# Performance work log

Hardware: AMD Instinct MI355X
Metric: run time of the kernel (lower is better)

Reference implementation:

```python
import jax, jax.numpy as jnp
import numpy as np

NUM_CLASSES = 80
NUM_ANCHORS = 9
NUM_CONVS = 4
FOCAL_ALPHA = 0.25
FOCAL_GAMMA = 2.0
LOSS_NORMALIZER = 100.0
LOSS_WEIGHT = 1.0
LEVEL_SHAPES = [(128, 128), (64, 64), (32, 32), (16, 16), (8, 8)]
C = 256
B = 2
N_TOTAL = NUM_ANCHORS * sum(h * w for h, w in LEVEL_SHAPES)  # 196416


def setup_inputs() -> dict:
    key = jax.random.key(0)
    ks = iter(jax.random.split(key, 32))
    inp = {}
    for i, (h, w) in enumerate(LEVEL_SHAPES):
        inp[f"feat{i}"] = jax.random.normal(next(ks), (B, h, w, C), dtype=jnp.float32)
    inp["anchor_labels"] = jax.random.randint(next(ks), (B, N_TOTAL), -1, NUM_CLASSES + 1, dtype=jnp.int32)
    inp["anchor_deltas"] = jax.random.normal(next(ks), (B, N_TOTAL, 4), dtype=jnp.float32)
    s = 0.05
    inp["in_proj_w"] = s * jax.random.normal(next(ks), (5, C, C), dtype=jnp.float32)  # [lvl, in, out]
    inp["in_proj_b"] = s * jax.random.normal(next(ks), (5, C), dtype=jnp.float32)
    inp["cls_convs_w"] = s * jax.random.normal(next(ks), (NUM_CONVS, 3, 3, C, C), dtype=jnp.float32)  # HWIO
    inp["cls_convs_b"] = s * jax.random.normal(next(ks), (NUM_CONVS, C), dtype=jnp.float32)
    inp["cls_score_w"] = s * jax.random.normal(next(ks), (3, 3, C, NUM_ANCHORS * NUM_CLASSES), dtype=jnp.float32)
    inp["cls_score_b"] = s * jax.random.normal(next(ks), (NUM_ANCHORS * NUM_CLASSES,), dtype=jnp.float32)
    inp["box_convs_w"] = s * jax.random.normal(next(ks), (NUM_CONVS, 3, 3, C, C), dtype=jnp.float32)
    inp["box_convs_b"] = s * jax.random.normal(next(ks), (NUM_CONVS, C), dtype=jnp.float32)
    inp["box_pred_w"] = s * jax.random.normal(next(ks), (3, 3, C, NUM_ANCHORS * 4), dtype=jnp.float32)
    inp["box_pred_b"] = s * jax.random.normal(next(ks), (NUM_ANCHORS * 4,), dtype=jnp.float32)
    return inp


def _conv(x, w, b):
    # x: [B,H,W,Cin] NHWC, w: [3,3,Cin,Cout] HWIO, stride 1, SAME padding
    y = jax.lax.conv_general_dilated(x, w, (1, 1), "SAME",
                                     dimension_numbers=("NHWC", "HWIO", "NHWC"))
    return y + b


def _head(feats, in_proj_w, in_proj_b, cls_convs_w, cls_convs_b, cls_score_w,
          cls_score_b, box_convs_w, box_convs_b, box_pred_w, box_pred_b):
    logit_maps, delta_maps = [], []
    for i, feat in enumerate(feats):  # fixed 5 FPN levels
        x = feat @ in_proj_w[i] + in_proj_b[i]  # in_proj Linear
        c = x
        for j in range(NUM_CONVS):
            c = jax.nn.relu(_conv(c, cls_convs_w[j], cls_convs_b[j]))
        logit = _conv(c, cls_score_w, cls_score_b)  # [B,H,W,A*K]
        d = x
        for j in range(NUM_CONVS):
            d = jax.nn.relu(_conv(d, box_convs_w[j], box_convs_b[j]))
        delta = _conv(d, box_pred_w, box_pred_b)  # [B,H,W,A*4]
        b, h, w, _ = logit.shape
        # reshape_pred_map: [B,H,W,A,P] -> [B, H*W*A, P] (channel c = a*P + p matches NHWC)
        logit_maps.append(logit.reshape(b, h * w * NUM_ANCHORS, NUM_CLASSES))
        delta_maps.append(delta.reshape(b, h * w * NUM_ANCHORS, 4))
    return jnp.concatenate(logit_maps, axis=1), jnp.concatenate(delta_maps, axis=1)


def reference(feat0, feat1, feat2, feat3, feat4, anchor_labels, anchor_deltas,
              in_proj_w, in_proj_b, cls_convs_w, cls_convs_b, cls_score_w,
              cls_score_b, box_convs_w, box_convs_b, box_pred_w, box_pred_b):
    logits, deltas = _head([feat0, feat1, feat2, feat3, feat4], in_proj_w,
                           in_proj_b, cls_convs_w, cls_convs_b, cls_score_w,
                           cls_score_b, box_convs_w, box_convs_b, box_pred_w,
                           box_pred_b)
    # classification: focal loss over anchors with label >= 0 (ignore label -1)
    class_mask = anchor_labels >= 0  # [B,N]
    safe_labels = jnp.where(class_mask, anchor_labels, NUM_CLASSES)
    targets = jax.nn.one_hot(safe_labels, NUM_CLASSES + 1, dtype=logits.dtype)[..., :NUM_CLASSES]
    # stable BCE-with-logits
    ce = jnp.maximum(logits, 0) - logits * targets + jnp.log1p(jnp.exp(-jnp.abs(logits)))
    p = jax.nn.sigmoid(logits)
    p_t = p * targets + (1 - p) * (1 - targets)
    loss = ce * (1 - p_t) ** FOCAL_GAMMA
    alpha_t = FOCAL_ALPHA * targets + (1 - FOCAL_ALPHA) * (1 - targets)
    loss = alpha_t * loss
    cls_loss = jnp.sum(loss * class_mask[..., None]) * (LOSS_WEIGHT / LOSS_NORMALIZER)
    box_mask = class_mask & (anchor_labels != NUM_CLASSES)
    l1 = jnp.abs(deltas - anchor_deltas)
    box_loss = jnp.sum(l1 * box_mask[..., None]) * (LOSS_WEIGHT / LOSS_NORMALIZER)
    return jnp.stack([cls_loss, box_loss])  # [ret_cls_loss, ret_box_loss]
```

## Files before the change

### kernel.cpp

```cpp
#include <hip/hip_runtime.h>
#include <hip/hip_bf16.h>

using bf16 = __hip_bfloat16;
typedef short short8 __attribute__((ext_vector_type(8)));
typedef short short4v __attribute__((ext_vector_type(4)));
typedef float f32x16 __attribute__((ext_vector_type(16)));

#define NT 196416

__device__ __forceinline__ void gload16(const void* g, void* l) {
  __builtin_amdgcn_global_load_lds((const __attribute__((address_space(1))) void*)g,
                                   (__attribute__((address_space(3))) void*)l, 16, 0, 0);
}

__global__ void prep_w(const float* __restrict__ src, bf16* __restrict__ dst,
                       int Cout, int NB, int TP, int layers, long sstride) {
  const long spl = (long)NB * 8 * 4 * TP * 64;
  const long total = spl * layers;
  for (long t = blockIdx.x * (long)blockDim.x + threadIdx.x; t < total;
       t += (long)gridDim.x * blockDim.x) {
    long layer = t / spl;
    long r = t - layer * spl;
    int nb = (int)(r / (2048L * TP));
    int r2 = (int)(r - (long)nb * 2048 * TP);
    int k = r2 / (256 * TP);
    int r3 = r2 - k * 256 * TP;
    int c = r3 / (64 * TP);
    int r4 = r3 - c * 64 * TP;
    int tap = r4 >> 6;
    int col = r4 & 63;
    int co = nb * 64 + col;
    short8 v = {};
    if (co < Cout) {
      const float* s = src + layer * sstride + ((long)(tap * 256 + k * 32 + c * 8)) * Cout + co;
#pragma unroll
      for (int j = 0; j < 8; ++j) {
        union { bf16 b; short s16; } u;
        u.b = __float2bfloat16(s[(long)j * Cout]);
        v[j] = u.s16;
      }
    }
    *(short8*)(dst + t * 8) = v;
  }
}

__global__ void halo3_kernel(bf16* __restrict__ base, long bufstride, int H, int W) {
  const int P = 2 * (W + 2) + 2 * H;
  const long n = 3L * 2 * P * 256;
  for (long t = blockIdx.x * (long)blockDim.x + threadIdx.x; t < n;
       t += (long)gridDim.x * blockDim.x) {
    int ch = (int)(t & 255);
    long q = t >> 8;
    int pix = (int)(q % P);
    int q2 = (int)(q / P);
    int img = q2 & 1;
    int buf = q2 >> 1;
    int row, col;
    if (pix < W + 2) { row = 0; col = pix; }
    else if (pix < 2 * (W + 2)) { row = H + 1; col = pix - (W + 2); }
    else { int e = pix - 2 * (W + 2); row = 1 + (e >> 1); col = (e & 1) ? W + 1 : 0; }
    bf16* p = base + buf * bufstride + ((long)(img * (H + 2) + row) * (W + 2) + col) * 256 + ch;
    union { bf16 b; short s16; } u; u.s16 = 0;
    *p = u.b;
  }
}

__global__ void cast_feat_kernel(const float* __restrict__ in, bf16* __restrict__ out,
                                 int H, int wshift) {
  const int W = 1 << wshift;
  const long n4 = 2L * H * W * 64;
  for (long t = blockIdx.x * (long)blockDim.x + threadIdx.x; t < n4;
       t += (long)gridDim.x * blockDim.x) {
    int c4 = (int)(t & 63);
    long q = t >> 6;
    int w = (int)(q & (W - 1));
    long q2 = q >> wshift;
    int h = (int)(q2 & (H - 1));
    int b = (int)(q2 >> wshift);
    const float4 f = *(const float4*)(in + (((long)(b * H + h) * W + w) * 256 + c4 * 4));
    short4v v;
    union { bf16 b16; short s16; } u;
    u.b16 = __float2bfloat16(f.x); v[0] = u.s16;
    u.b16 = __float2bfloat16(f.y); v[1] = u.s16;
    u.b16 = __float2bfloat16(f.z); v[2] = u.s16;
    u.b16 = __float2bfloat16(f.w); v[3] = u.s16;
    *(short4v*)(out + (((long)(b * (H + 2) + h + 1) * (W + 2) + w + 1) * 256 + c4 * 4)) = v;
  }
}

template <int BM, int WM, int WN, int TAPS, int EPI, int PM>
__global__ __launch_bounds__(WM * WN * 64, 4) void conv_t(
    const bf16* __restrict__ in, const bf16* __restrict__ wp,
    const float* __restrict__ bias, bf16* __restrict__ outp,
    int H, int wshift, const int* __restrict__ labels,
    const float* __restrict__ tdel, int abase, float* __restrict__ lout, int Cout) {
  constexpr int BLOCK = WM * WN * 64;
  constexpr int MF = BM / WM / 32;
  constexpr int NROW = TAPS * 64;
  constexpr int BOFF = 64 * PM;
  constexpr int NB_SLOTS = TAPS * 256;
  constexpr int CG = BLOCK / 4;

  __shared__ char smem[64 * PM + TAPS * 4096];

  const int W = 1 << wshift;
  const int tid = threadIdx.x;
  const int lane = tid & 63;
  const int wid = tid >> 6;
  const int wm = wid / WN;
  const int wn = wid % WN;
  const int lh = lane >> 5;
  const int l31 = lane & 31;

  const int R = BM >> wshift;
  const int PP = (R + 2) * (W + 2);
  const int img = blockIdx.z;
  const int rb = blockIdx.x;
  const int n0 = blockIdx.y * 64;
  const int W2_16 = (W + 2) * 16;

  int aOff[MF];
#pragma unroll
  for (int mf = 0; mf < MF; ++mf) {
    const int mrow = wm * (BM / WM) + mf * 32 + l31;
    const int pb = (mrow >> wshift) * (W + 2) + (mrow & (W - 1));
    aOff[mf] = (lh * PP + pb) * 16;
  }
  const int bOff = (lh * NROW + wn * 32 + l31) * 16;

  const int cst = tid / CG;
  const int lig = tid - cst * CG;
  const int wib = tid & ~63;
  const int ldsA_base = (cst * PP + (wib % CG)) * 16;
  const bf16* gA = in + ((long)(img * (H + 2) + rb * R) * (W + 2)) * 256 + cst * 8;
  const bf16* gB = wp + ((long)blockIdx.y * TAPS * 2048 + tid) * 8;
  const int nkk = (PP + CG - 1) / CG;

  f32x16 acc[MF];
#pragma unroll
  for (int mf = 0; mf < MF; ++mf) acc[mf] = (f32x16)(0.f);

  for (int k = 0; k < 8; ++k) {
    __syncthreads();
    for (int kk = 0; kk < nkk; ++kk) {
      const int p = kk * CG + lig;
      if (p < PP)
        gload16(gA + (long)p * 256 + k * 32, smem + ldsA_base + kk * CG * 16);
    }
#pragma unroll
    for (int s0 = 0; s0 < NB_SLOTS; s0 += BLOCK) {
      if (s0 + tid < NB_SLOTS)
        gload16(gB + ((long)k * NB_SLOTS + s0) * 8, smem + BOFF + (s0 + wib) * 16);
    }
    __syncthreads();
#pragma unroll
    for (int t = 0; t < TAPS; ++t) {
      int toff;
      if (TAPS == 9) toff = (t / 3) * W2_16 + (t % 3) * 16;
      else toff = W2_16 + 16;
      const short8 b0 = *(const short8*)(smem + BOFF + bOff + t * 1024);
      const short8 b1 = *(const short8*)(smem + BOFF + bOff + NROW * 32 + t * 1024);
#pragma unroll
      for (int mf = 0; mf < MF; ++mf) {
        const short8 a0 = *(const short8*)(smem + aOff[mf] + toff);
        const short8 a1 = *(const short8*)(smem + aOff[mf] + PP * 32 + toff);
        acc[mf] = __builtin_amdgcn_mfma_f32_32x32x16_bf16(a0, b0, acc[mf], 0, 0, 0);
        acc[mf] = __builtin_amdgcn_mfma_f32_32x32x16_bf16(a1, b1, acc[mf], 0, 0, 0);
      }
    }
  }

  const int co = n0 + wn * 32 + l31;

  if constexpr (EPI == 0) {
    const float bv = bias[co];
#pragma unroll
    for (int mf = 0; mf < MF; ++mf) {
#pragma unroll
      for (int r = 0; r < 16; ++r) {
        const int mrow = wm * (BM / WM) + mf * 32 + (r & 3) + 8 * (r >> 2) + 4 * lh;
        const int rr = rb * BM + mrow;
        const int h = rr >> wshift;
        const int w = rr & (W - 1);
        float v = acc[mf][r] + bv;
        if (TAPS == 9) v = fmaxf(v, 0.f);
        outp[((long)(img * (H + 2) + h + 1) * (W + 2) + w + 1) * 256 + co] = __float2bfloat16(v);
      }
    }
  } else {
    float lsum = 0.f;
    const bool valid = co < Cout;
    const float bv = valid ? bias[co] : 0.f;
    int aidx = 0, sub = 0;
    if constexpr (EPI == 1) { aidx = co / 80; sub = co - aidx * 80; }
    else { aidx = co >> 2; sub = co & 3; }
    if (valid) {
#pragma unroll
      for (int mf = 0; mf < MF; ++mf) {
#pragma unroll
        for (int r = 0; r < 16; ++r) {
          const int mrow = wm * (BM / WM) + mf * 32 + (r & 3) + 8 * (r >> 2) + 4 * lh;
          const int rr = rb * BM + mrow;
          const int idx = abase + rr * 9 + aidx;
          const int label = labels[(long)img * NT + idx];
          const float z = acc[mf][r] + bv;
          if constexpr (EPI == 1) {
            if (label >= 0) {
              const float tt = (label == sub) ? 1.f : 0.f;
              const float ce = fmaxf(z, 0.f) - z * tt + log1pf(expf(-fabsf(z)));
              const float p = 1.f / (1.f + expf(-z));
              const float pt = p * tt + (1.f - p) * (1.f - tt);
              const float om = 1.f - pt;
              lsum += (0.25f * tt + 0.75f * (1.f - tt)) * ce * om * om;
            }
          } else {
            if (label >= 0 && label != 80) {
              lsum += fabsf(z - tdel[((long)img * NT + idx) * 4 + sub]);
            }
          }
        }
      }
    }
#pragma unroll
    for (int off = 32; off > 0; off >>= 1) lsum += __shfl_down(lsum, off, 64);
    __syncthreads();
    float* red = (float*)smem;
    if (lane == 0) red[wid] = lsum;
    __syncthreads();
    if (tid == 0) {
      float s = 0.f;
      for (int i = 0; i < BLOCK / 64; ++i) s += red[i];
      atomicAdd(lout, s * 0.01f);
    }
  }
}


struct Ctx {
  const bf16 *wip, *wcls, *wbox, *wsc, *wpred;
  const float *ipb, *ccb, *csb, *bcb, *bpb;
  const int* labels;
  const float* tdel;
  bf16 *xb, *t0, *t1;
  float* out;
};

template <int BM, int WM, int WN, int PM>
static void run_level(const Ctx& P, int H, int wshift, int abase, hipStream_t s) {
  const int W = 1 << wshift;
  const int mpb = H * W / BM;
  dim3 blk(WM * WN * 64);
  conv_t<BM, WM, WN, 1, 0, PM><<<dim3(mpb, 4, 2), blk, 0, s>>>(
      P.t0, P.wip, P.ipb, P.xb, H, wshift, nullptr, nullptr, 0, nullptr, 256);
  bf16* pp[2] = {P.t0, P.t1};
  const bf16* cin = P.xb;
  for (int j = 0; j < 4; ++j) {
    conv_t<BM, WM, WN, 9, 0, PM><<<dim3(mpb, 4, 2), blk, 0, s>>>(
        cin, P.wcls + (long)j * 589824, P.ccb + j * 256, pp[j & 1], H, wshift,
        nullptr, nullptr, 0, nullptr, 256);
    cin = pp[j & 1];
  }
  conv_t<BM, WM, WN, 9, 1, PM><<<dim3(mpb, 12, 2), blk, 0, s>>>(
      cin, P.wsc, P.csb, nullptr, H, wshift, P.labels, nullptr, abase, P.out + 0, 720);
  cin = P.xb;
  for (int j = 0; j < 4; ++j) {
    conv_t<BM, WM, WN, 9, 0, PM><<<dim3(mpb, 4, 2), blk, 0, s>>>(
        cin, P.wbox + (long)j * 589824, P.bcb + j * 256, pp[j & 1], H, wshift,
        nullptr, nullptr, 0, nullptr, 256);
    cin = pp[j & 1];
  }
  conv_t<BM, WM, WN, 9, 2, PM><<<dim3(mpb, 1, 2), blk, 0, s>>>(
      cin, P.wpred, P.bpb, nullptr, H, wshift, P.labels, P.tdel, abase, P.out + 1, 36);
}

static inline int igrid(long n, int cap) {
  long g = (n + 255) / 256;
  return (int)(g > cap ? cap : g);
}

extern "C" void kernel_launch(void* const* d_in, const int* in_sizes, int n_in,
                              void* d_out, int out_size, void* d_ws, size_t ws_size,
                              hipStream_t stream) {
  const float* feat_in[5] = {(const float*)d_in[0], (const float*)d_in[1],
                             (const float*)d_in[2], (const float*)d_in[3],
                             (const float*)d_in[4]};
  const int* labels = (const int*)d_in[5];
  const float* adeltas = (const float*)d_in[6];
  const float* ipw = (const float*)d_in[7];
  const float* ipb = (const float*)d_in[8];
  const float* ccw = (const float*)d_in[9];
  const float* ccb = (const float*)d_in[10];
  const float* csw = (const float*)d_in[11];
  const float* csb = (const float*)d_in[12];
  const float* bcw = (const float*)d_in[13];
  const float* bcb = (const float*)d_in[14];
  const float* bpw = (const float*)d_in[15];
  const float* bpb = (const float*)d_in[16];
  float* out = (float*)d_out;

  const long BUF = 8652800;
  bf16* ws = (bf16*)d_ws;
  bf16* xb = ws;
  bf16* t0 = ws + BUF;
  bf16* t1 = ws + 2 * BUF;
  bf16* wp_ip = ws + 3 * BUF;
  bf16* wp_cls = wp_ip + 327680;
  bf16* wp_box = wp_cls + 2359296;
  bf16* wp_sc = wp_box + 2359296;
  bf16* wp_pred = wp_sc + 1769472;

  hipMemsetAsync(d_out, 0, 2 * sizeof(float), stream);

  prep_w<<<igrid(5L * 8192, 2048), 256, 0, stream>>>(ipw, wp_ip, 256, 4, 1, 5, 65536);
  prep_w<<<igrid(4L * 73728, 2048), 256, 0, stream>>>(ccw, wp_cls, 256, 4, 9, 4, 589824);
  prep_w<<<igrid(4L * 73728, 2048), 256, 0, stream>>>(bcw, wp_box, 256, 4, 9, 4, 589824);
  prep_w<<<igrid(221184L, 2048), 256, 0, stream>>>(csw, wp_sc, 720, 12, 9, 1, 0);
  prep_w<<<igrid(18432L, 2048), 256, 0, stream>>>(bpw, wp_pred, 36, 1, 9, 1, 0);

  static const int LH[5] = {128, 64, 32, 16, 8};
  static const int LS[5] = {7, 6, 5, 4, 3};
  static const int AB[5] = {0, 147456, 184320, 193536, 195840};

  Ctx P;
  P.wcls = wp_cls; P.wbox = wp_box; P.wsc = wp_sc; P.wpred = wp_pred;
  P.ccb = ccb; P.csb = csb; P.bcb = bcb; P.bpb = bpb;
  P.labels = labels; P.tdel = adeltas;
  P.xb = xb; P.t0 = t0; P.t1 = t1; P.out = out;

  for (int l = 0; l < 5; ++l) {
    const int H = LH[l], wsh = LS[l];
    P.wip = wp_ip + (long)l * 65536;
    P.ipb = ipb + l * 256;
    halo3_kernel<<<igrid(3L * 2 * (2 * (H + 2 + H)) * 256, 2048), 256, 0, stream>>>(
        xb, BUF, H, H);
    cast_feat_kernel<<<igrid(2L * H * H * 64, 2048), 256, 0, stream>>>(
        feat_in[l], t0, H, wsh);
    switch (l) {
      case 0: run_level<256, 4, 2, 520>(P, H, wsh, AB[l], stream); break;
      case 1: run_level<128, 2, 2, 264>(P, H, wsh, AB[l], stream); break;
      case 2: run_level<128, 2, 2, 264>(P, H, wsh, AB[l], stream); break;
      case 3: run_level<128, 2, 2, 264>(P, H, wsh, AB[l], stream); break;
      case 4: run_level<64, 2, 2, 100>(P, H, wsh, AB[l], stream); break;
    }
  }
}
```

Measured before the change: 1.666 ms.

## Rewrite conv kernel with 128-wide N tiles, double buffering, and merged cls/box launches

The conv kernel is rebuilt. Each block now covers 128 output channels with two N fragments per wave, the K loop moves to 16-channel chunks, and smaller levels can double-buffer their LDS stages using manual vmcnt waits and barriers. When the workspace is large enough, the cls and box tower convs run in one launch via a split grid. Labels and deltas are staged in LDS for the loss epilogue, and the weight packing layout and per-level tile shapes change to match. This aims to cut launch count, improve reuse of the A tile across more output channels, and overlap loads with MFMA, at the cost of more LDS, lower occupancy and new padding and layout assumptions.

```diff
diff --git a/kernel.cpp b/kernel.cpp
--- a/kernel.cpp
+++ b/kernel.cpp
@@ -8,45 +8,47 @@
 
 #define NT 196416
 
-__device__ __forceinline__ void gload16(const void* g, void* l) {
+__device__ __forceinline__ void gload16(const bf16* g, char* l) {
   __builtin_amdgcn_global_load_lds((const __attribute__((address_space(1))) void*)g,
                                    (__attribute__((address_space(3))) void*)l, 16, 0, 0);
 }
 
+template <int N> __device__ __forceinline__ void vmw() {
+  asm volatile("s_waitcnt vmcnt(%0)" ::"n"(N) : "memory");
+}
+
 __global__ void prep_w(const float* __restrict__ src, bf16* __restrict__ dst,
-                       int Cout, int NB, int TP, int layers, long sstride) {
-  const long spl = (long)NB * 8 * 4 * TP * 64;
+                       int Cout, int NB, int TAPS, int layers, long sstride) {
+  const long spl = (long)NB * 16 * 2 * TAPS * 128;
   const long total = spl * layers;
-  for (long t = blockIdx.x * (long)blockDim.x + threadIdx.x; t < total;
-       t += (long)gridDim.x * blockDim.x) {
-    long layer = t / spl;
-    long r = t - layer * spl;
-    int nb = (int)(r / (2048L * TP));
-    int r2 = (int)(r - (long)nb * 2048 * TP);
-    int k = r2 / (256 * TP);
-    int r3 = r2 - k * 256 * TP;
-    int c = r3 / (64 * TP);
-    int r4 = r3 - c * 64 * TP;
-    int tap = r4 >> 6;
-    int col = r4 & 63;
-    int co = nb * 64 + col;
+  for (long s = blockIdx.x * (long)blockDim.x + threadIdx.x; s < total;
+       s += (long)gridDim.x * blockDim.x) {
+    long layer = s / spl;
+    long r = s - layer * spl;
+    int col = (int)(r & 127);
+    long q = r >> 7;
+    int t = (int)(q % TAPS); q /= TAPS;
+    int c = (int)(q & 1); q >>= 1;
+    int k = (int)(q & 15);
+    int nb = (int)(q >> 4);
+    int co = nb * 128 + col;
     short8 v = {};
     if (co < Cout) {
-      const float* s = src + layer * sstride + ((long)(tap * 256 + k * 32 + c * 8)) * Cout + co;
+      const float* p = src + layer * sstride + ((long)(t * 256 + k * 16 + c * 8)) * Cout + co;
 #pragma unroll
       for (int j = 0; j < 8; ++j) {
         union { bf16 b; short s16; } u;
-        u.b = __float2bfloat16(s[(long)j * Cout]);
+        u.b = __float2bfloat16(p[(long)j * Cout]);
         v[j] = u.s16;
       }
     }
-    *(short8*)(dst + t * 8) = v;
-  }
-}
-
-__global__ void halo3_kernel(bf16* __restrict__ base, long bufstride, int H, int W) {
-  const int P = 2 * (W + 2) + 2 * H;
-  const long n = 3L * 2 * P * 256;
+    *(short8*)(dst + s * 8) = v;
+  }
+}
+
+__global__ void halo_kernel(bf16* __restrict__ base, long BS, int W, int nbuf) {
+  const int P = 2 * (W + 2) + 2 * W;
+  const long n = (long)nbuf * 2 * P * 256;
   for (long t = blockIdx.x * (long)blockDim.x + threadIdx.x; t < n;
        t += (long)gridDim.x * blockDim.x) {
     int ch = (int)(t & 255);
@@ -57,165 +59,231 @@
     int buf = q2 >> 1;
     int row, col;
     if (pix < W + 2) { row = 0; col = pix; }
-    else if (pix < 2 * (W + 2)) { row = H + 1; col = pix - (W + 2); }
+    else if (pix < 2 * (W + 2)) { row = W + 1; col = pix - (W + 2); }
     else { int e = pix - 2 * (W + 2); row = 1 + (e >> 1); col = (e & 1) ? W + 1 : 0; }
-    bf16* p = base + buf * bufstride + ((long)(img * (H + 2) + row) * (W + 2) + col) * 256 + ch;
+    bf16* p = base + buf * BS + ((long)(img * (W + 2) + row) * (W + 2) + col) * 256 + ch;
     union { bf16 b; short s16; } u; u.s16 = 0;
     *p = u.b;
   }
 }
 
 __global__ void cast_feat_kernel(const float* __restrict__ in, bf16* __restrict__ out,
-                                 int H, int wshift) {
+                                 int wshift) {
   const int W = 1 << wshift;
-  const long n4 = 2L * H * W * 64;
+  const long n4 = 2L * W * W * 64;
   for (long t = blockIdx.x * (long)blockDim.x + threadIdx.x; t < n4;
        t += (long)gridDim.x * blockDim.x) {
     int c4 = (int)(t & 63);
     long q = t >> 6;
     int w = (int)(q & (W - 1));
     long q2 = q >> wshift;
-    int h = (int)(q2 & (H - 1));
+    int h = (int)(q2 & (W - 1));
     int b = (int)(q2 >> wshift);
-    const float4 f = *(const float4*)(in + (((long)(b * H + h) * W + w) * 256 + c4 * 4));
+    const float4 f = *(const float4*)(in + (((long)(b * W + h) * W + w) * 256 + c4 * 4));
     short4v v;
     union { bf16 b16; short s16; } u;
     u.b16 = __float2bfloat16(f.x); v[0] = u.s16;
     u.b16 = __float2bfloat16(f.y); v[1] = u.s16;
     u.b16 = __float2bfloat16(f.z); v[2] = u.s16;
     u.b16 = __float2bfloat16(f.w); v[3] = u.s16;
-    *(short4v*)(out + (((long)(b * (H + 2) + h + 1) * (W + 2) + w + 1) * 256 + c4 * 4)) = v;
-  }
-}
-
-template <int BM, int WM, int WN, int TAPS, int EPI, int PM>
-__global__ __launch_bounds__(WM * WN * 64, 4) void conv_t(
-    const bf16* __restrict__ in, const bf16* __restrict__ wp,
-    const float* __restrict__ bias, bf16* __restrict__ outp,
-    int H, int wshift, const int* __restrict__ labels,
-    const float* __restrict__ tdel, int abase, float* __restrict__ lout, int Cout) {
-  constexpr int BLOCK = WM * WN * 64;
-  constexpr int MF = BM / WM / 32;
-  constexpr int NROW = TAPS * 64;
-  constexpr int BOFF = 64 * PM;
-  constexpr int NB_SLOTS = TAPS * 256;
-  constexpr int CG = BLOCK / 4;
-
-  __shared__ char smem[64 * PM + TAPS * 4096];
-
-  const int W = 1 << wshift;
+    *(short4v*)(out + (((long)(b * (W + 2) + h + 1) * (W + 2) + w + 1) * 256 + c4 * 4)) = v;
+  }
+}
+
+template <int WSH, int WM, int WN, int MFR, int TAPS, int EPI, int DBUF>
+__global__ __launch_bounds__(WM * WN * 64, 2) void conv_t(
+    const bf16* __restrict__ inA, const bf16* __restrict__ inB,
+    const bf16* __restrict__ wpA, const bf16* __restrict__ wpB,
+    const float* __restrict__ biasA, const float* __restrict__ biasB,
+    bf16* __restrict__ outA, bf16* __restrict__ outB,
+    const int* __restrict__ labels, const float* __restrict__ tdel,
+    int abase, float* __restrict__ lout, int Cout, int nbHalf) {
+  constexpr int W = 1 << WSH;
+  constexpr int NW = WM * WN;
+  constexpr int BM = WM * MFR * 32;
+  constexpr int R = BM >> WSH;
+  constexpr int PP = (R + 2) * (W + 2);
+  constexpr int PPA0 = ((PP + 63) / 64) * 64;
+  constexpr int PPA = (NW == 4 && (PPA0 % 128)) ? PPA0 + 64 : PPA0;
+  constexpr int PG = PPA / 64;
+  constexpr int UA = PPA / 32;
+  constexpr int UB = TAPS * 4;
+  constexpr int U = UA + UB;
+  static_assert(U % NW == 0, "unit padding");
+  constexpr int UPW = U / NW;
+  constexpr int ABYTES = 2 * PPA * 16;
+  constexpr int BUFB = ABYTES + TAPS * 4096;
+
+  __shared__ __align__(16) char smem[BUFB * (DBUF ? 2 : 1)];
+
   const int tid = threadIdx.x;
   const int lane = tid & 63;
   const int wid = tid >> 6;
   const int wm = wid / WN;
   const int wn = wid % WN;
+  const int l31 = lane & 31;
   const int lh = lane >> 5;
-  const int l31 = lane & 31;
-
-  const int R = BM >> wshift;
-  const int PP = (R + 2) * (W + 2);
+
+  const int yb = blockIdx.y;
+  const int half = (yb >= nbHalf) ? 1 : 0;
+  const int nb = yb - half * nbHalf;
+  const int n0 = nb * 128;
+  const int rb = blockIdx.x;
   const int img = blockIdx.z;
-  const int rb = blockIdx.x;
-  const int n0 = blockIdx.y * 64;
-  const int W2_16 = (W + 2) * 16;
-
-  int aOff[MF];
-#pragma unroll
-  for (int mf = 0; mf < MF; ++mf) {
-    const int mrow = wm * (BM / WM) + mf * 32 + l31;
-    const int pb = (mrow >> wshift) * (W + 2) + (mrow & (W - 1));
-    aOff[mf] = (lh * PP + pb) * 16;
-  }
-  const int bOff = (lh * NROW + wn * 32 + l31) * 16;
-
-  const int cst = tid / CG;
-  const int lig = tid - cst * CG;
-  const int wib = tid & ~63;
-  const int ldsA_base = (cst * PP + (wib % CG)) * 16;
-  const bf16* gA = in + ((long)(img * (H + 2) + rb * R) * (W + 2)) * 256 + cst * 8;
-  const bf16* gB = wp + ((long)blockIdx.y * TAPS * 2048 + tid) * 8;
-  const int nkk = (PP + CG - 1) / CG;
-
-  f32x16 acc[MF];
-#pragma unroll
-  for (int mf = 0; mf < MF; ++mf) acc[mf] = (f32x16)(0.f);
-
-  for (int k = 0; k < 8; ++k) {
+
+  const bf16* in = half ? inB : inA;
+  const bf16* wp = half ? wpB : wpA;
+  const float* bias = half ? biasB : biasA;
+  bf16* outp = half ? outB : outA;
+
+  const bf16* gA = in + (long)(img * (W + 2) + rb * R) * ((W + 2) * 256);
+  const bf16* gB = wp + (long)nb * (TAPS * 32768);
+
+  int a16[MFR];
+#pragma unroll
+  for (int mf = 0; mf < MFR; ++mf) {
+    const int mrow = wm * (MFR * 32) + mf * 32 + l31;
+    const int pb = (mrow >> WSH) * (W + 2) + (mrow & (W - 1));
+    a16[mf] = (lh * PPA + pb) * 16;
+  }
+  int b16[2];
+#pragma unroll
+  for (int nf = 0; nf < 2; ++nf)
+    b16[nf] = ABYTES + (lh * (TAPS * 128) + wn * 64 + nf * 32 + l31) * 16;
+
+  f32x16 acc[MFR][2];
+#pragma unroll
+  for (int mf = 0; mf < MFR; ++mf) {
+    acc[mf][0] = (f32x16)(0.f);
+    acc[mf][1] = (f32x16)(0.f);
+  }
+
+  auto STAGE = [&](int cc, char* ldsb) {
+#pragma unroll
+    for (int i = 0; i < UPW; ++i) {
+      const int u = wid + NW * i;
+      if (u < UA) {
+        const int cg = (u >= PG) ? 1 : 0;
+        const int pu = (u - cg * PG) * 64;
+        gload16(gA + ((long)(pu + lane) * 256 + cg * 8 + cc * 16),
+                ldsb + (cg * PPA + pu) * 16);
+      } else {
+        const int s0 = (u - UA) * 64;
+        gload16(gB + (long)cc * (TAPS * 2048) + (s0 + lane) * 8,
+                ldsb + ABYTES + s0 * 16);
+      }
+    }
+  };
+
+  auto COMPUTE = [&](const char* ldsb) {
+#pragma unroll
+    for (int t = 0; t < TAPS; ++t) {
+      const int TOFF = (TAPS == 9) ? (((t / 3) * (W + 2) + (t % 3)) * 16)
+                                   : ((W + 3) * 16);
+      short8 bfr[2];
+#pragma unroll
+      for (int nf = 0; nf < 2; ++nf)
+        bfr[nf] = *(const short8*)(ldsb + b16[nf] + t * 2048);
+#pragma unroll
+      for (int mf = 0; mf < MFR; ++mf) {
+        const short8 afr = *(const short8*)(ldsb + a16[mf] + TOFF);
+        acc[mf][0] = __builtin_amdgcn_mfma_f32_32x32x16_bf16(afr, bfr[0], acc[mf][0], 0, 0, 0);
+        acc[mf][1] = __builtin_amdgcn_mfma_f32_32x32x16_bf16(afr, bfr[1], acc[mf][1], 0, 0, 0);
+      }
+    }
+  };
+
+  if constexpr (DBUF) {
+    char* bb0 = smem;
+    char* bb1 = smem + BUFB;
+    STAGE(0, bb0);
+#pragma unroll 1
+    for (int i = 0; i < 8; ++i) {
+      STAGE(2 * i + 1, bb1);
+      vmw<UPW>();
+      __builtin_amdgcn_s_barrier();
+      COMPUTE(bb0);
+      __builtin_amdgcn_s_barrier();
+      if (i < 7) {
+        STAGE(2 * i + 2, bb0);
+        vmw<UPW>();
+      } else {
+        vmw<0>();
+      }
+      __builtin_amdgcn_s_barrier();
+      COMPUTE(bb1);
+      __builtin_amdgcn_s_barrier();
+    }
+  } else {
+#pragma unroll 1
+    for (int cc = 0; cc < 16; ++cc) {
+      __syncthreads();
+      STAGE(cc, smem);
+      __syncthreads();
+      COMPUTE(smem);
+    }
+  }
+
+  if constexpr (EPI == 0) {
+#pragma unroll
+    for (int nf = 0; nf < 2; ++nf) {
+      const int co = n0 + wn * 64 + nf * 32 + l31;
+      const float bv = bias[co];
+#pragma unroll
+      for (int mf = 0; mf < MFR; ++mf) {
+#pragma unroll
+        for (int r = 0; r < 16; ++r) {
+          const int mrow = wm * (MFR * 32) + mf * 32 + (r & 3) + 8 * (r >> 2) + 4 * lh;
+          const int rr = rb * BM + mrow;
+          const int h = rr >> WSH;
+          const int w = rr & (W - 1);
+          float v = acc[mf][nf][r] + bv;
+          if (TAPS == 9) v = fmaxf(v, 0.f);
+          outp[((long)(img * (W + 2) + h + 1) * (W + 2) + (w + 1)) * 256 + co] =
+              __float2bfloat16(v);
+        }
+      }
+    }
+  } else {
     __syncthreads();
-    for (int kk = 0; kk < nkk; ++kk) {
-      const int p = kk * CG + lig;
-      if (p < PP)
-        gload16(gA + (long)p * 256 + k * 32, smem + ldsA_base + kk * CG * 16);
-    }
-#pragma unroll
-    for (int s0 = 0; s0 < NB_SLOTS; s0 += BLOCK) {
-      if (s0 + tid < NB_SLOTS)
-        gload16(gB + ((long)k * NB_SLOTS + s0) * 8, smem + BOFF + (s0 + wib) * 16);
+    int* lsh = (int*)smem;
+    float* dsh = (float*)(smem + BM * 9 * 4);
+    const long lbase = (long)img * NT + abase + (long)rb * BM * 9;
+    for (int i = tid; i < BM * 9; i += NW * 64) lsh[i] = labels[lbase + i];
+    if constexpr (EPI == 2) {
+      for (int i = tid; i < BM * 9 * 4; i += NW * 64) dsh[i] = tdel[lbase * 4 + i];
     }
     __syncthreads();
-#pragma unroll
-    for (int t = 0; t < TAPS; ++t) {
-      int toff;
-      if (TAPS == 9) toff = (t / 3) * W2_16 + (t % 3) * 16;
-      else toff = W2_16 + 16;
-      const short8 b0 = *(const short8*)(smem + BOFF + bOff + t * 1024);
-      const short8 b1 = *(const short8*)(smem + BOFF + bOff + NROW * 32 + t * 1024);
-#pragma unroll
-      for (int mf = 0; mf < MF; ++mf) {
-        const short8 a0 = *(const short8*)(smem + aOff[mf] + toff);
-        const short8 a1 = *(const short8*)(smem + aOff[mf] + PP * 32 + toff);
-        acc[mf] = __builtin_amdgcn_mfma_f32_32x32x16_bf16(a0, b0, acc[mf], 0, 0, 0);
-        acc[mf] = __builtin_amdgcn_mfma_f32_32x32x16_bf16(a1, b1, acc[mf], 0, 0, 0);
-      }
-    }
-  }
-
-  const int co = n0 + wn * 32 + l31;
-
-  if constexpr (EPI == 0) {
-    const float bv = bias[co];
-#pragma unroll
-    for (int mf = 0; mf < MF; ++mf) {
-#pragma unroll
-      for (int r = 0; r < 16; ++r) {
-        const int mrow = wm * (BM / WM) + mf * 32 + (r & 3) + 8 * (r >> 2) + 4 * lh;
-        const int rr = rb * BM + mrow;
-        const int h = rr >> wshift;
-        const int w = rr & (W - 1);
-        float v = acc[mf][r] + bv;
-        if (TAPS == 9) v = fmaxf(v, 0.f);
-        outp[((long)(img * (H + 2) + h + 1) * (W + 2) + w + 1) * 256 + co] = __float2bfloat16(v);
-      }
-    }
-  } else {
+
     float lsum = 0.f;
-    const bool valid = co < Cout;
-    const float bv = valid ? bias[co] : 0.f;
-    int aidx = 0, sub = 0;
-    if constexpr (EPI == 1) { aidx = co / 80; sub = co - aidx * 80; }
-    else { aidx = co >> 2; sub = co & 3; }
-    if (valid) {
-#pragma unroll
-      for (int mf = 0; mf < MF; ++mf) {
-#pragma unroll
-        for (int r = 0; r < 16; ++r) {
-          const int mrow = wm * (BM / WM) + mf * 32 + (r & 3) + 8 * (r >> 2) + 4 * lh;
-          const int rr = rb * BM + mrow;
-          const int idx = abase + rr * 9 + aidx;
-          const int label = labels[(long)img * NT + idx];
-          const float z = acc[mf][r] + bv;
-          if constexpr (EPI == 1) {
-            if (label >= 0) {
-              const float tt = (label == sub) ? 1.f : 0.f;
-              const float ce = fmaxf(z, 0.f) - z * tt + log1pf(expf(-fabsf(z)));
-              const float p = 1.f / (1.f + expf(-z));
-              const float pt = p * tt + (1.f - p) * (1.f - tt);
-              const float om = 1.f - pt;
-              lsum += (0.25f * tt + 0.75f * (1.f - tt)) * ce * om * om;
-            }
-          } else {
-            if (label >= 0 && label != 80) {
-              lsum += fabsf(z - tdel[((long)img * NT + idx) * 4 + sub]);
+#pragma unroll
+    for (int nf = 0; nf < 2; ++nf) {
+      const int co = n0 + wn * 64 + nf * 32 + l31;
+      if (co < Cout) {
+        const float bv = bias[co];
+        int aidx, sub;
+        if constexpr (EPI == 1) { aidx = co / 80; sub = co - aidx * 80; }
+        else { aidx = co >> 2; sub = co & 3; }
+#pragma unroll
+        for (int mf = 0; mf < MFR; ++mf) {
+#pragma unroll
+          for (int r = 0; r < 16; ++r) {
+            const int mrow = wm * (MFR * 32) + mf * 32 + (r & 3) + 8 * (r >> 2) + 4 * lh;
+            const int label = lsh[mrow * 9 + aidx];
+            const float z = acc[mf][nf][r] + bv;
+            if constexpr (EPI == 1) {
+              if (label >= 0) {
+                const float tt = (label == sub) ? 1.f : 0.f;
+                const float ce = fmaxf(z, 0.f) - z * tt + log1pf(expf(-fabsf(z)));
+                const float p = 1.f / (1.f + expf(-z));
+                const float pt = p * tt + (1.f - p) * (1.f - tt);
+                const float om = 1.f - pt;
+                lsum += (0.25f * tt + 0.75f * (1.f - tt)) * ce * om * om;
+              }
+            } else {
+              if (label >= 0 && label != 80) {
+                lsum += fabsf(z - dsh[(mrow * 9 + aidx) * 4 + sub]);
+              }
             }
           }
         }
@@ -229,53 +297,82 @@
     __syncthreads();
     if (tid == 0) {
       float s = 0.f;
-      for (int i = 0; i < BLOCK / 64; ++i) s += red[i];
+      for (int i = 0; i < NW; ++i) s += red[i];
       atomicAdd(lout, s * 0.01f);
     }
   }
-}
-
-
-struct Ctx {
-  const bf16 *wip, *wcls, *wbox, *wsc, *wpred;
-  const float *ipb, *ccb, *csb, *bcb, *bpb;
-  const int* labels;
-  const float* tdel;
-  bf16 *xb, *t0, *t1;
-  float* out;
-};
-
-template <int BM, int WM, int WN, int PM>
-static void run_level(const Ctx& P, int H, int wshift, int abase, hipStream_t s) {
-  const int W = 1 << wshift;
-  const int mpb = H * W / BM;
-  dim3 blk(WM * WN * 64);
-  conv_t<BM, WM, WN, 1, 0, PM><<<dim3(mpb, 4, 2), blk, 0, s>>>(
-      P.t0, P.wip, P.ipb, P.xb, H, wshift, nullptr, nullptr, 0, nullptr, 256);
-  bf16* pp[2] = {P.t0, P.t1};
-  const bf16* cin = P.xb;
-  for (int j = 0; j < 4; ++j) {
-    conv_t<BM, WM, WN, 9, 0, PM><<<dim3(mpb, 4, 2), blk, 0, s>>>(
-        cin, P.wcls + (long)j * 589824, P.ccb + j * 256, pp[j & 1], H, wshift,
-        nullptr, nullptr, 0, nullptr, 256);
-    cin = pp[j & 1];
-  }
-  conv_t<BM, WM, WN, 9, 1, PM><<<dim3(mpb, 12, 2), blk, 0, s>>>(
-      cin, P.wsc, P.csb, nullptr, H, wshift, P.labels, nullptr, abase, P.out + 0, 720);
-  cin = P.xb;
-  for (int j = 0; j < 4; ++j) {
-    conv_t<BM, WM, WN, 9, 0, PM><<<dim3(mpb, 4, 2), blk, 0, s>>>(
-        cin, P.wbox + (long)j * 589824, P.bcb + j * 256, pp[j & 1], H, wshift,
-        nullptr, nullptr, 0, nullptr, 256);
-    cin = pp[j & 1];
-  }
-  conv_t<BM, WM, WN, 9, 2, PM><<<dim3(mpb, 1, 2), blk, 0, s>>>(
-      cin, P.wpred, P.bpb, nullptr, H, wshift, P.labels, P.tdel, abase, P.out + 1, 36);
 }
 
 static inline int igrid(long n, int cap) {
   long g = (n + 255) / 256;
   return (int)(g > cap ? cap : g);
+}
+
+struct LvlArgs {
+  bf16* bufs; long BS;
+  const bf16 *wip, *wcls, *wbox, *wsc, *wpred;
+  const float *ipb, *ccb, *csb, *bcb, *bpb;
+  const int* labels; const float* tdel;
+  int abase; float* out;
+};
+
+template <int WSH, int WM, int WN, int MFR, int TDB>
+static void run_level(const LvlArgs& A, bool merged, hipStream_t s) {
+  constexpr int W = 1 << WSH;
+  constexpr int BM = WM * MFR * 32;
+  const int m = (W * W) / BM;
+  dim3 blk(WM * WN * 64);
+  if (merged) {
+    bf16* xb = A.bufs;
+    bf16* c0 = A.bufs + A.BS;
+    bf16* c1 = A.bufs + 2 * A.BS;
+    bf16* d0 = A.bufs + 3 * A.BS;
+    bf16* d1 = A.bufs + 4 * A.BS;
+    conv_t<WSH, WM, WN, MFR, 1, 0, 1><<<dim3(m, 2, 2), blk, 0, s>>>(
+        c1, c1, A.wip, A.wip, A.ipb, A.ipb, xb, xb, nullptr, nullptr, 0, nullptr, 256, 2);
+    const bf16* ci = xb; const bf16* bi = xb;
+    bf16* co_[4] = {c0, c1, c0, c1};
+    bf16* bo_[4] = {d0, d1, d0, d1};
+    for (int j = 0; j < 4; ++j) {
+      conv_t<WSH, WM, WN, MFR, 9, 0, TDB><<<dim3(m, 4, 2), blk, 0, s>>>(
+          ci, bi, A.wcls + (long)j * 589824, A.wbox + (long)j * 589824,
+          A.ccb + j * 256, A.bcb + j * 256, co_[j], bo_[j],
+          nullptr, nullptr, 0, nullptr, 256, 2);
+      ci = co_[j]; bi = bo_[j];
+    }
+    conv_t<WSH, WM, WN, MFR, 9, 1, TDB><<<dim3(m, 6, 2), blk, 0, s>>>(
+        ci, ci, A.wsc, A.wsc, A.csb, A.csb, nullptr, nullptr,
+        A.labels, nullptr, A.abase, A.out + 0, 720, 6);
+    conv_t<WSH, WM, WN, MFR, 9, 2, TDB><<<dim3(m, 1, 2), blk, 0, s>>>(
+        bi, bi, A.wpred, A.wpred, A.bpb, A.bpb, nullptr, nullptr,
+        A.labels, A.tdel, A.abase, A.out + 1, 36, 1);
+  } else {
+    bf16* xb = A.bufs;
+    bf16* t0 = A.bufs + A.BS;
+    bf16* t1 = A.bufs + 2 * A.BS;
+    conv_t<WSH, WM, WN, MFR, 1, 0, 1><<<dim3(m, 2, 2), blk, 0, s>>>(
+        t0, t0, A.wip, A.wip, A.ipb, A.ipb, xb, xb, nullptr, nullptr, 0, nullptr, 256, 2);
+    for (int br = 0; br < 2; ++br) {
+      const bf16* wt = br ? A.wbox : A.wcls;
+      const float* bb = br ? A.bcb : A.ccb;
+      const bf16* ci = xb;
+      bf16* oo[4] = {t1, t0, t1, t0};
+      for (int j = 0; j < 4; ++j) {
+        conv_t<WSH, WM, WN, MFR, 9, 0, TDB><<<dim3(m, 2, 2), blk, 0, s>>>(
+            ci, ci, wt + (long)j * 589824, wt + (long)j * 589824, bb + j * 256, bb + j * 256,
+            oo[j], oo[j], nullptr, nullptr, 0, nullptr, 256, 2);
+        ci = oo[j];
+      }
+      if (br == 0)
+        conv_t<WSH, WM, WN, MFR, 9, 1, TDB><<<dim3(m, 6, 2), blk, 0, s>>>(
+            t0, t0, A.wsc, A.wsc, A.csb, A.csb, nullptr, nullptr,
+            A.labels, nullptr, A.abase, A.out + 0, 720, 6);
+      else
+        conv_t<WSH, WM, WN, MFR, 9, 2, TDB><<<dim3(m, 1, 2), blk, 0, s>>>(
+            t0, t0, A.wpred, A.wpred, A.bpb, A.bpb, nullptr, nullptr,
+            A.labels, A.tdel, A.abase, A.out + 1, 36, 1);
+    }
+  }
 }
 
 extern "C" void kernel_launch(void* const* d_in, const int* in_sizes, int n_in,
@@ -298,12 +395,15 @@
   const float* bpb = (const float*)d_in[16];
   float* out = (float*)d_out;
 
-  const long BUF = 8652800;
+  const long BUFE = 2L * 130 * 130 * 256;
+  const long GAP = 65536;
+  const long BS = BUFE + GAP;
+  const long WELEMS = 327680 + 2359296 + 2359296 + 1769472 + 294912;
+  const bool merged = ws_size >= (size_t)((5 * BS + WELEMS) * 2);
+  const int nbuf = merged ? 5 : 3;
+
   bf16* ws = (bf16*)d_ws;
-  bf16* xb = ws;
-  bf16* t0 = ws + BUF;
-  bf16* t1 = ws + 2 * BUF;
-  bf16* wp_ip = ws + 3 * BUF;
+  bf16* wp_ip = ws + nbuf * BS;
   bf16* wp_cls = wp_ip + 327680;
   bf16* wp_box = wp_cls + 2359296;
   bf16* wp_sc = wp_box + 2359296;
@@ -311,36 +411,37 @@
 
   hipMemsetAsync(d_out, 0, 2 * sizeof(float), stream);
 
-  prep_w<<<igrid(5L * 8192, 2048), 256, 0, stream>>>(ipw, wp_ip, 256, 4, 1, 5, 65536);
-  prep_w<<<igrid(4L * 73728, 2048), 256, 0, stream>>>(ccw, wp_cls, 256, 4, 9, 4, 589824);
-  prep_w<<<igrid(4L * 73728, 2048), 256, 0, stream>>>(bcw, wp_box, 256, 4, 9, 4, 589824);
-  prep_w<<<igrid(221184L, 2048), 256, 0, stream>>>(csw, wp_sc, 720, 12, 9, 1, 0);
-  prep_w<<<igrid(18432L, 2048), 256, 0, stream>>>(bpw, wp_pred, 36, 1, 9, 1, 0);
-
-  static const int LH[5] = {128, 64, 32, 16, 8};
+  prep_w<<<igrid(5L * 8192, 1024), 256, 0, stream>>>(ipw, wp_ip, 256, 2, 1, 5, 65536);
+  prep_w<<<igrid(4L * 73728, 1024), 256, 0, stream>>>(ccw, wp_cls, 256, 2, 9, 4, 589824);
+  prep_w<<<igrid(4L * 73728, 1024), 256, 0, stream>>>(bcw, wp_box, 256, 2, 9, 4, 589824);
+  prep_w<<<igrid(221184L, 1024), 256, 0, stream>>>(csw, wp_sc, 720, 6, 9, 1, 0);
+  prep_w<<<igrid(36864L, 1024), 256, 0, stream>>>(bpw, wp_pred, 36, 1, 9, 1, 0);
+
   static const int LS[5] = {7, 6, 5, 4, 3};
   static const int AB[5] = {0, 147456, 184320, 193536, 195840};
 
-  Ctx P;
-  P.wcls = wp_cls; P.wbox = wp_box; P.wsc = wp_sc; P.wpred = wp_pred;
-  P.ccb = ccb; P.csb = csb; P.bcb = bcb; P.bpb = bpb;
-  P.labels = labels; P.tdel = adeltas;
-  P.xb = xb; P.t0 = t0; P.t1 = t1; P.out = out;
+  bf16* featsBuf = ws + (merged ? 2 : 1) * BS;
 
   for (int l = 0; l < 5; ++l) {
-    const int H = LH[l], wsh = LS[l];
-    P.wip = wp_ip + (long)l * 65536;
-    P.ipb = ipb + l * 256;
-    halo3_kernel<<<igrid(3L * 2 * (2 * (H + 2 + H)) * 256, 2048), 256, 0, stream>>>(
-        xb, BUF, H, H);
-    cast_feat_kernel<<<igrid(2L * H * H * 64, 2048), 256, 0, stream>>>(
-        feat_in[l], t0, H, wsh);
+    const int W = 1 << LS[l];
+    halo_kernel<<<igrid((long)nbuf * 2 * (4 * W + 4) * 256, 2048), 256, 0, stream>>>(
+        ws, BS, W, nbuf);
+    cast_feat_kernel<<<igrid(2L * W * W * 64, 2048), 256, 0, stream>>>(
+        feat_in[l], featsBuf, LS[l]);
+
+    LvlArgs A;
+    A.bufs = ws; A.BS = BS;
+    A.wip = wp_ip + (long)l * 65536; A.ipb = ipb + l * 256;
+    A.wcls = wp_cls; A.wbox = wp_box; A.wsc = wp_sc; A.wpred = wp_pred;
+    A.ccb = ccb; A.csb = csb; A.bcb = bcb; A.bpb = bpb;
+    A.labels = labels; A.tdel = adeltas; A.abase = AB[l]; A.out = out;
+
     switch (l) {
-      case 0: run_level<256, 4, 2, 520>(P, H, wsh, AB[l], stream); break;
-      case 1: run_level<128, 2, 2, 264>(P, H, wsh, AB[l], stream); break;
-      case 2: run_level<128, 2, 2, 264>(P, H, wsh, AB[l], stream); break;
-      case 3: run_level<128, 2, 2, 264>(P, H, wsh, AB[l], stream); break;
-      case 4: run_level<64, 2, 2, 100>(P, H, wsh, AB[l], stream); break;
-    }
-  }
-}
+      case 0: run_level<7, 2, 2, 4, 0>(A, merged, stream); break;
+      case 1: run_level<6, 2, 2, 2, 1>(A, merged, stream); break;
+      case 2: run_level<5, 1, 2, 2, 1>(A, merged, stream); break;
+      case 3: run_level<4, 1, 2, 2, 1>(A, merged, stream); break;
+      case 4: run_level<3, 1, 2, 2, 1>(A, merged, stream); break;
+    }
+  }
+}
```

Result: slower. 1.788 ms (+7.3%).
